# Performance work log

Measured on AMD Instinct MI355X. Metric: run time of the kernel, lower is better.

Reference implementation:

```python
import jax, jax.numpy as jnp
import numpy as np

# Structural hyperparams (mirror init_kwargs)
G, Q, C, D = 2, 8, 1024, 8          # groups, quantizers/group, codebook_size, codebook_dim
DIMS = 1024                          # residual_fsq.dim
DPG = DIMS // G                      # dim per group (project_out output)
B, L = 4, 4096                       # batch, frame length
UP_K, UP_S = 4, 2                    # upsample ConvTranspose1d kernel/stride
HEAD_K, HEAD_OUT = 7, 512            # head Conv1d kernel / out channels


def setup_inputs() -> dict:
    key = jax.random.key(0)
    ks = jax.random.split(key, 8)
    indices = jax.random.randint(ks[0], (B, G * Q, L), 0, C, dtype=jnp.int64)
    codebooks = jax.random.normal(ks[1], (G, Q, C, D), jnp.float32)
    scales = jax.random.uniform(ks[2], (G, Q, D), jnp.float32, 0.5, 2.0)
    W_out = jax.random.normal(ks[3], (G, D, DPG), jnp.float32) * (1.0 / np.sqrt(D))
    b_out = jnp.zeros((G, DPG), jnp.float32)
    W_up = jax.random.normal(ks[4], (DIMS, DIMS, UP_K), jnp.float32) * 0.02   # IOH layout
    b_up = jnp.zeros((DIMS,), jnp.float32)
    W_head = jax.random.normal(ks[5], (HEAD_OUT, DIMS, HEAD_K), jnp.float32) * 0.02  # OIH
    b_head = jnp.zeros((HEAD_OUT,), jnp.float32)
    return dict(indices=indices, codebooks=codebooks, scales=scales,
                W_out=W_out, b_out=b_out, W_up=W_up, b_up=b_up,
                W_head=W_head, b_head=b_head)


def reference(indices, codebooks, scales, W_out, b_out, W_up, b_up, W_head, b_head):
    b, gq, l = indices.shape
    g, q = codebooks.shape[0], codebooks.shape[1]
    # [B, G*Q, L] -> [G, B, L, Q]  (matches view + permute in forward)
    idx = indices.reshape(b, g, q, l).transpose(1, 0, 3, 2)
    mask = idx == -1                              # dropout-padded codes
    idx0 = jnp.where(mask, 0, idx)
    # gather codes per (group, quantizer): codebooks[g, q, idx0[g,b,l,q]] -> [G,B,L,Q,D]
    g_ix = jnp.arange(g)[:, None, None, None]
    q_ix = jnp.arange(q)[None, None, None, :]
    codes = codebooks[g_ix, q_ix, idx0]
    # mask, scale, sum over quantizers (residual sum)
    codes = jnp.where(mask[..., None], 0.0, codes) * scales[:, None, None, :, :]
    summed = codes.sum(axis=3)                    # [G,B,L,D]
    # per-group project_out: Linear(D -> DPG)
    z = jnp.einsum('gbld,gde->gble', summed, W_out) + b_out[:, None, None, :]
    # concat groups along feature dim -> [B, L, DIMS], then NCH for convs
    z_q = z.transpose(1, 2, 0, 3).reshape(b, l, g * z.shape[-1])
    zc = z_q.transpose(0, 2, 1)                   # [B, DIMS, L]
    # upsample: ConvTranspose1d(DIMS->DIMS, k=4, stride=2) -> [B, DIMS, 2L]
    zu = jax.lax.conv_transpose(zc, W_up, strides=(UP_S,), padding='SAME',
                                dimension_numbers=('NCH', 'IOH', 'NCH'))
    zu = zu + b_up[None, :, None]
    # head: Conv1d(DIMS -> HEAD_OUT, k=7, same padding)
    x = jax.lax.conv_general_dilated(zu, W_head, window_strides=(1,), padding='SAME',
                                     dimension_numbers=('NCH', 'OIH', 'NCH'))
    x = x + b_head[None, :, None]
    return x
```

## Files before the change

### kernel.cpp

```cpp
#include <hip/hip_runtime.h>
#include <hip/hip_bf16.h>

typedef __attribute__((ext_vector_type(8))) short bf16x8;
typedef __attribute__((ext_vector_type(4))) float f32x4;

#define GQ 16
#define L_IN 4096
#define T_UP 8192
#define CB 1024
#define ZROWS 4098
#define UROWS 8198

__device__ __forceinline__ void gload16(const void* g, void* l) {
    __builtin_amdgcn_global_load_lds((const __attribute__((address_space(1))) void*)g,
                                     (__attribute__((address_space(3))) void*)l, 16, 0, 0);
}

#define SB()  __builtin_amdgcn_s_barrier()
#define LGKM() do { asm volatile("s_waitcnt lgkmcnt(0)" ::: "memory"); \
                    __builtin_amdgcn_sched_barrier(0); } while (0)
#define VMW(n) do { __builtin_amdgcn_sched_barrier(0); \
                    asm volatile("s_waitcnt vmcnt(" #n ")" ::: "memory"); \
                    __builtin_amdgcn_sched_barrier(0); } while (0)

#define MM(MH, NH) do {                                                          \
    __builtin_amdgcn_s_setprio(1);                                               \
    _Pragma("unroll") for (int j_ = 0; j_ < 4; ++j_)                             \
      _Pragma("unroll") for (int n_ = 0; n_ < 2; ++n_)                           \
        _Pragma("unroll") for (int s_ = 0; s_ < 2; ++s_)                         \
          acc[(MH)*4 + j_][(NH)*2 + n_] = __builtin_amdgcn_mfma_f32_16x16x32_bf16( \
              af[j_][s_], bq[(NH)*2 + n_][s_], acc[(MH)*4 + j_][(NH)*2 + n_],    \
              0, 0, 0);                                                          \
    __builtin_amdgcn_s_setprio(0);                                               \
} while (0)

__global__ __launch_bounds__(256) void zero_pads(__hip_bfloat16* __restrict__ zp,
                                                 __hip_bfloat16* __restrict__ zup) {
    int idx = blockIdx.x * 256 + threadIdx.x;
    if (idx < 8192) {
        int b = idx >> 11, rs = (idx >> 10) & 1, c = idx & 1023;
        size_t row = (size_t)b * ZROWS + (rs ? (ZROWS - 1) : 0);
        zp[row * 1024 + c] = __float2bfloat16(0.f);
    } else if (idx < 8192 + 24576) {
        int rem = idx - 8192;
        int b = rem / 6144, r2 = rem % 6144;
        int r6 = r2 >> 10, c = r2 & 1023;
        size_t row = (size_t)b * UROWS + (r6 < 3 ? r6 : (UROWS - 6 + r6));
        zup[row * 1024 + c] = __float2bfloat16(0.f);
    }
}

__global__ __launch_bounds__(256) void repack_up(const float* __restrict__ Wup,
                                                 __hip_bfloat16* __restrict__ Wr) {
    int idx = blockIdx.x * 256 + threadIdx.x;
    int kk = idx >> 20;
    int co = (idx >> 10) & 1023;
    int ci = idx & 1023;
    Wr[idx] = __float2bfloat16(Wup[((ci << 10) + co) * 4 + kk]);
}

__global__ __launch_bounds__(256) void repack_head(const float* __restrict__ Wh,
                                                   __hip_bfloat16* __restrict__ Wr) {
    int idx = blockIdx.x * 256 + threadIdx.x;
    int kk = idx >> 19;
    int rem = idx & ((1 << 19) - 1);
    int o = rem >> 10;
    int ci = rem & 1023;
    Wr[idx] = __float2bfloat16(Wh[(o * 1024 + ci) * 7 + kk]);
}

__global__ __launch_bounds__(256) void dequant_project(
    const int* __restrict__ indices, const float* __restrict__ codebooks,
    const float* __restrict__ scales, const float* __restrict__ Wout,
    const float* __restrict__ bout, __hip_bfloat16* __restrict__ z)
{
    __shared__ float w_lds[8192];
    __shared__ float b_lds[1024];
    __shared__ float part[128];
    __shared__ float summed[16];
    int tid = threadIdx.x;
    for (int k = tid; k < 8192; k += 256) w_lds[k] = Wout[k];
    for (int k = tid; k < 1024; k += 256) b_lds[k] = bout[k];
    int p0 = blockIdx.x * 16;
    int b  = p0 >> 12;
    int l0 = p0 & 4095;
    __syncthreads();
    for (int i = 0; i < 16; ++i) {
        int l = l0 + i;
        if (tid < 128) {
            int gq = tid >> 3;
            int d  = tid & 7;
            int idx = indices[(b * GQ + gq) * L_IN + l];
            float v = 0.f;
            if (idx >= 0) {
                int ic = (idx < CB) ? idx : 0;
                v = codebooks[(gq * CB + ic) * 8 + d] * scales[gq * 8 + d];
            }
            part[tid] = v;
        }
        __syncthreads();
        if (tid < 16) {
            int g = tid >> 3, d = tid & 7;
            float s = 0.f;
            for (int q = 0; q < 8; ++q) s += part[(g * 8 + q) * 8 + d];
            summed[tid] = s;
        }
        __syncthreads();
        #pragma unroll
        for (int j = 0; j < 4; ++j) {
            int c = tid + j * 256;
            int g = c >> 9;
            float acc = b_lds[c];
            #pragma unroll
            for (int d = 0; d < 8; ++d)
                acc += summed[g * 8 + d] * w_lds[(g * 8 + d) * 512 + (c & 511)];
            z[((size_t)b * ZROWS + l + 1) * 1024 + c] = __float2bfloat16(acc);
        }
        __syncthreads();
    }
}


__global__ __launch_bounds__(512, 2) void conv_up_mfma(
    const __hip_bfloat16* __restrict__ zp, const __hip_bfloat16* __restrict__ Wr,
    const float* __restrict__ bup, __hip_bfloat16* __restrict__ zup)
{
    __shared__ __hip_bfloat16 Als[2][256][64];
    __shared__ __hip_bfloat16 Bls[2][256][64];
    const int tid = threadIdx.x;
    const int lane = tid & 63;
    const int w = tid >> 6;
    const int wm = w >> 2, wn = w & 3;
    const int l15 = lane & 15, kq = lane >> 4;
    const int m0  = blockIdx.x * 256;
    const int co0 = blockIdx.y * 256;
    const int b = blockIdx.z >> 1, P = blockIdx.z & 1;
    const int NT = 32, NIT = 16;

    const __hip_bfloat16* abase = zp + ((size_t)b * ZROWS + m0 + P) * 1024;
    const __hip_bfloat16* bbase = Wr + ((size_t)P * 1024 + co0) * 1024;

    auto stage = [&](int kt, int part) {
        if (kt >= NT) return;
        const int buf = kt & 1;
        const int j = kt >> 4, ci0 = (kt & 15) << 6;
        const int rb = (part & 1) << 7;
        const __hip_bfloat16* src;
        __hip_bfloat16* dst;
        if (part < 2) { src = abase + ((size_t)j + rb) * 1024 + ci0;
                        dst = &Als[buf][rb][0]; }
        else          { src = bbase + ((size_t)j * 2048 + rb) * 1024 + ci0;
                        dst = &Bls[buf][rb][0]; }
        #pragma unroll
        for (int it = 0; it < 2; ++it) {
            int chunk = it * 512 + tid;
            int row = chunk >> 3, cs = chunk & 7;
            int cq = cs ^ (row & 7);
            gload16(src + (size_t)row * 1024 + cq * 8,
                    (char*)dst + ((it * 512 + (w << 6)) << 4));
        }
    };

    f32x4 acc[8][4];
    const f32x4 z4 = {0.f, 0.f, 0.f, 0.f};
    #pragma unroll
    for (int i = 0; i < 8; ++i)
        #pragma unroll
        for (int j = 0; j < 4; ++j) acc[i][j] = z4;

    bf16x8 af[4][2], bq[4][2];

    auto rdA = [&](int buf, int mh) {
        #pragma unroll
        for (int j = 0; j < 4; ++j)
            #pragma unroll
            for (int sl = 0; sl < 2; ++sl) {
                int row = (wm << 7) + (mh << 6) + j * 16 + l15;
                int ch = (sl * 4 + kq) ^ (row & 7);
                af[j][sl] = *(const bf16x8*)&Als[buf][row][ch * 8];
            }
    };
    auto rdB = [&](int buf) {
        #pragma unroll
        for (int nf = 0; nf < 4; ++nf)
            #pragma unroll
            for (int sl = 0; sl < 2; ++sl) {
                int row = (wn << 6) + nf * 16 + l15;
                int ch = (sl * 4 + kq) ^ (row & 7);
                bq[nf][sl] = *(const bf16x8*)&Bls[buf][row][ch * 8];
            }
    };

    stage(0, 2); stage(0, 3); stage(0, 0); stage(0, 1);
    stage(1, 2); stage(1, 3); stage(1, 0);
    VMW(6);
    SB();

    for (int it = 0; it < NIT; ++it) {
        const bool lastit = (it == NIT - 1);
        rdA(0, 0); rdB(0);
        stage(2 * it + 1, 1);
        SB(); LGKM(); MM(0, 0); SB();
        stage(2 * it + 2, 2);
        SB(); MM(0, 1); SB();
        rdA(0, 1);
        stage(2 * it + 2, 3);
        SB(); LGKM(); MM(1, 1); SB();
        stage(2 * it + 2, 0);
        if (lastit) { VMW(0); } else { VMW(6); }
        SB(); MM(1, 0); SB();
        rdA(1, 0); rdB(1);
        stage(2 * it + 2, 1);
        SB(); LGKM(); MM(0, 0); SB();
        stage(2 * it + 3, 2);
        SB(); MM(0, 1); SB();
        rdA(1, 1);
        stage(2 * it + 3, 3);
        SB(); LGKM(); MM(1, 1); SB();
        stage(2 * it + 3, 0);
        if (!lastit) { VMW(6); }
        SB(); MM(1, 0); SB();
    }

    float bias[4];
    #pragma unroll
    for (int nf = 0; nf < 4; ++nf) bias[nf] = bup[co0 + (wn << 6) + nf * 16 + l15];
    const int mbase = m0 + (wm << 7) + (kq << 2);
    const int cob = co0 + (wn << 6) + l15;
    #pragma unroll
    for (int mf = 0; mf < 8; ++mf)
        #pragma unroll
        for (int e = 0; e < 4; ++e) {
            int m = mbase + mf * 16 + e;
            size_t rowoff = ((size_t)b * UROWS + 3 + P + 2 * m) * 1024;
            #pragma unroll
            for (int nf = 0; nf < 4; ++nf)
                zup[rowoff + cob + nf * 16] = __float2bfloat16(acc[mf][nf][e] + bias[nf]);
        }
}

__global__ __launch_bounds__(512, 2) void conv_head_mfma(
    const __hip_bfloat16* __restrict__ zup, const __hip_bfloat16* __restrict__ Wr,
    const float* __restrict__ bh, float* __restrict__ out)
{
    __shared__ __hip_bfloat16 Als[2][256][64];
    __shared__ __hip_bfloat16 Bls[2][256][64];
    const int tid = threadIdx.x;
    const int lane = tid & 63;
    const int w = tid >> 6;
    const int wm = w >> 2, wn = w & 3;
    const int l15 = lane & 15, kq = lane >> 4;
    const int t0 = blockIdx.x * 256;
    const int o0 = blockIdx.y * 256;
    const int b  = blockIdx.z;
    const int NT = 112, NIT = 56;

    const __hip_bfloat16* bbase = zup + ((size_t)b * UROWS + t0) * 1024;

    auto stage = [&](int kt, int part) {
        if (kt >= NT) return;
        const int buf = kt & 1;
        const int kk = kt >> 4, ci0 = (kt & 15) << 6;
        const int rb = (part & 1) << 7;
        const __hip_bfloat16* src;
        __hip_bfloat16* dst;
        if (part < 2) { src = Wr + ((size_t)(kk * 512 + o0 + rb)) * 1024 + ci0;
                        dst = &Als[buf][rb][0]; }
        else          { src = bbase + ((size_t)(kk + rb)) * 1024 + ci0;
                        dst = &Bls[buf][rb][0]; }
        #pragma unroll
        for (int it = 0; it < 2; ++it) {
            int chunk = it * 512 + tid;
            int row = chunk >> 3, cs = chunk & 7;
            int cq = cs ^ (row & 7);
            gload16(src + (size_t)row * 1024 + cq * 8,
                    (char*)dst + ((it * 512 + (w << 6)) << 4));
        }
    };

    f32x4 acc[8][4];
    const f32x4 z4 = {0.f, 0.f, 0.f, 0.f};
    #pragma unroll
    for (int i = 0; i < 8; ++i)
        #pragma unroll
        for (int j = 0; j < 4; ++j) acc[i][j] = z4;

    bf16x8 af[4][2], bq[4][2];

    auto rdA = [&](int buf, int mh) {
        #pragma unroll
        for (int j = 0; j < 4; ++j)
            #pragma unroll
            for (int sl = 0; sl < 2; ++sl) {
                int row = (wm << 7) + (mh << 6) + j * 16 + l15;
                int ch = (sl * 4 + kq) ^ (row & 7);
                af[j][sl] = *(const bf16x8*)&Als[buf][row][ch * 8];
            }
    };
    auto rdB = [&](int buf) {
        #pragma unroll
        for (int nf = 0; nf < 4; ++nf)
            #pragma unroll
            for (int sl = 0; sl < 2; ++sl) {
                int row = (wn << 6) + nf * 16 + l15;
                int ch = (sl * 4 + kq) ^ (row & 7);
                bq[nf][sl] = *(const bf16x8*)&Bls[buf][row][ch * 8];
            }
    };

    stage(0, 2); stage(0, 3); stage(0, 0); stage(0, 1);
    stage(1, 2); stage(1, 3); stage(1, 0);
    VMW(6);
    SB();

    for (int it = 0; it < NIT; ++it) {
        const bool lastit = (it == NIT - 1);
        rdA(0, 0); rdB(0);
        stage(2 * it + 1, 1);
        SB(); LGKM(); MM(0, 0); SB();
        stage(2 * it + 2, 2);
        SB(); MM(0, 1); SB();
        rdA(0, 1);
        stage(2 * it + 2, 3);
        SB(); LGKM(); MM(1, 1); SB();
        stage(2 * it + 2, 0);
        if (lastit) { VMW(0); } else { VMW(6); }
        SB(); MM(1, 0); SB();
        rdA(1, 0); rdB(1);
        stage(2 * it + 2, 1);
        SB(); LGKM(); MM(0, 0); SB();
        stage(2 * it + 3, 2);
        SB(); MM(0, 1); SB();
        rdA(1, 1);
        stage(2 * it + 3, 3);
        SB(); LGKM(); MM(1, 1); SB();
        stage(2 * it + 3, 0);
        if (!lastit) { VMW(6); }
        SB(); MM(1, 0); SB();
    }

    const int obase = o0 + (wm << 7) + (kq << 2);
    const int tbase = t0 + (wn << 6) + l15;
    #pragma unroll
    for (int mf = 0; mf < 8; ++mf)
        #pragma unroll
        for (int e = 0; e < 4; ++e) {
            int o = obase + mf * 16 + e;
            float bias = bh[o];
            size_t rowoff = ((size_t)b * 512 + o) * T_UP + tbase;
            #pragma unroll
            for (int nf = 0; nf < 4; ++nf)
                out[rowoff + nf * 16] = acc[mf][nf][e] + bias;
        }
}

extern "C" void kernel_launch(void* const* d_in, const int* in_sizes, int n_in,
                              void* d_out, int out_size, void* d_ws, size_t ws_size,
                              hipStream_t stream) {
    const int*   indices   = (const int*)d_in[0];
    const float* codebooks = (const float*)d_in[1];
    const float* scales    = (const float*)d_in[2];
    const float* Wout      = (const float*)d_in[3];
    const float* bout      = (const float*)d_in[4];
    const float* Wup       = (const float*)d_in[5];
    const float* bup       = (const float*)d_in[6];
    const float* Wh        = (const float*)d_in[7];
    const float* bh        = (const float*)d_in[8];
    float* out = (float*)d_out;

    __hip_bfloat16* zp    = (__hip_bfloat16*)d_ws;
    __hip_bfloat16* zup   = zp + (size_t)4 * ZROWS * 1024;
    __hip_bfloat16* wr_up = zup + (size_t)4 * UROWS * 1024;
    __hip_bfloat16* wr_h  = wr_up + (size_t)4 * 1024 * 1024;

    zero_pads  <<<dim3(128),   dim3(256), 0, stream>>>(zp, zup);
    repack_up  <<<dim3(16384), dim3(256), 0, stream>>>(Wup, wr_up);
    repack_head<<<dim3(14336), dim3(256), 0, stream>>>(Wh, wr_h);
    dequant_project<<<dim3(1024), dim3(256), 0, stream>>>(indices, codebooks, scales,
                                                          Wout, bout, zp);
    conv_up_mfma  <<<dim3(16, 4, 8), dim3(512), 0, stream>>>(zp, wr_up, bup, zup);
    conv_head_mfma<<<dim3(32, 2, 4), dim3(512), 0, stream>>>(zup, wr_h, bh, out);
}
```

Before: 466.6 us.

## Interleave LDS fragment reads with MFMA phases in both conv GEMM loops

Splits the B-fragment LDS reads into low and high halves and issues the next fragment reads right after each MFMA block, inside the barrier window, instead of before the block that needs them. The intent is to overlap LDS read latency with matrix-core work in the upsample and head GEMM loops. Barriers are wrapped in compiler scheduling fences so the compiler cannot move memory operations across them. This adds scheduling constraints and register-liveness pressure, and there is a risk of reading LDS data while another wave is still overwriting it.

```diff
diff --git a/kernel.cpp b/kernel.cpp
--- a/kernel.cpp
+++ b/kernel.cpp
@@ -16,7 +16,11 @@
                                      (__attribute__((address_space(3))) void*)l, 16, 0, 0);
 }
 
-#define SB()  __builtin_amdgcn_s_barrier()
+#define SBR() do { asm volatile("" ::: "memory");                 \
+                   __builtin_amdgcn_sched_barrier(0);             \
+                   __builtin_amdgcn_s_barrier();                  \
+                   __builtin_amdgcn_sched_barrier(0);             \
+                   asm volatile("" ::: "memory"); } while (0)
 #define LGKM() do { asm volatile("s_waitcnt lgkmcnt(0)" ::: "memory"); \
                     __builtin_amdgcn_sched_barrier(0); } while (0)
 #define VMW(n) do { __builtin_amdgcn_sched_barrier(0); \
@@ -180,9 +184,19 @@
                 af[j][sl] = *(const bf16x8*)&Als[buf][row][ch * 8];
             }
     };
-    auto rdB = [&](int buf) {
-        #pragma unroll
-        for (int nf = 0; nf < 4; ++nf)
+    auto rdBlo = [&](int buf) {
+        #pragma unroll
+        for (int nf = 0; nf < 2; ++nf)
+            #pragma unroll
+            for (int sl = 0; sl < 2; ++sl) {
+                int row = (wn << 6) + nf * 16 + l15;
+                int ch = (sl * 4 + kq) ^ (row & 7);
+                bq[nf][sl] = *(const bf16x8*)&Bls[buf][row][ch * 8];
+            }
+    };
+    auto rdBhi = [&](int buf) {
+        #pragma unroll
+        for (int nf = 2; nf < 4; ++nf)
             #pragma unroll
             for (int sl = 0; sl < 2; ++sl) {
                 int row = (wn << 6) + nf * 16 + l15;
@@ -194,32 +208,51 @@
     stage(0, 2); stage(0, 3); stage(0, 0); stage(0, 1);
     stage(1, 2); stage(1, 3); stage(1, 0);
     VMW(6);
-    SB();
+    SBR();
+    rdA(0, 0); rdBlo(0);
 
     for (int it = 0; it < NIT; ++it) {
         const bool lastit = (it == NIT - 1);
-        rdA(0, 0); rdB(0);
         stage(2 * it + 1, 1);
-        SB(); LGKM(); MM(0, 0); SB();
+        SBR(); LGKM();
+        MM(0, 0);
+        rdBhi(0);
+        SBR();
         stage(2 * it + 2, 2);
-        SB(); MM(0, 1); SB();
+        SBR(); LGKM();
+        MM(0, 1);
         rdA(0, 1);
+        SBR();
         stage(2 * it + 2, 3);
-        SB(); LGKM(); MM(1, 1); SB();
+        SBR(); LGKM();
+        MM(1, 1);
+        SBR();
         stage(2 * it + 2, 0);
         if (lastit) { VMW(0); } else { VMW(6); }
-        SB(); MM(1, 0); SB();
-        rdA(1, 0); rdB(1);
+        SBR();
+        MM(1, 0);
+        rdA(1, 0); rdBlo(1);
+        SBR();
         stage(2 * it + 2, 1);
-        SB(); LGKM(); MM(0, 0); SB();
+        SBR(); LGKM();
+        MM(0, 0);
+        rdBhi(1);
+        SBR();
         stage(2 * it + 3, 2);
-        SB(); MM(0, 1); SB();
+        SBR(); LGKM();
+        MM(0, 1);
         rdA(1, 1);
+        SBR();
         stage(2 * it + 3, 3);
-        SB(); LGKM(); MM(1, 1); SB();
+        SBR(); LGKM();
+        MM(1, 1);
+        SBR();
         stage(2 * it + 3, 0);
         if (!lastit) { VMW(6); }
-        SB(); MM(1, 0); SB();
+        SBR();
+        MM(1, 0);
+        if (!lastit) { rdA(0, 0); rdBlo(0); }
+        SBR();
     }
 
     float bias[4];
@@ -297,9 +330,19 @@
                 af[j][sl] = *(const bf16x8*)&Als[buf][row][ch * 8];
             }
     };
-    auto rdB = [&](int buf) {
-        #pragma unroll
-        for (int nf = 0; nf < 4; ++nf)
+    auto rdBlo = [&](int buf) {
+        #pragma unroll
+        for (int nf = 0; nf < 2; ++nf)
+            #pragma unroll
+            for (int sl = 0; sl < 2; ++sl) {
+                int row = (wn << 6) + nf * 16 + l15;
+                int ch = (sl * 4 + kq) ^ (row & 7);
+                bq[nf][sl] = *(const bf16x8*)&Bls[buf][row][ch * 8];
+            }
+    };
+    auto rdBhi = [&](int buf) {
+        #pragma unroll
+        for (int nf = 2; nf < 4; ++nf)
             #pragma unroll
             for (int sl = 0; sl < 2; ++sl) {
                 int row = (wn << 6) + nf * 16 + l15;
@@ -311,32 +354,51 @@
     stage(0, 2); stage(0, 3); stage(0, 0); stage(0, 1);
     stage(1, 2); stage(1, 3); stage(1, 0);
     VMW(6);
-    SB();
+    SBR();
+    rdA(0, 0); rdBlo(0);
 
     for (int it = 0; it < NIT; ++it) {
         const bool lastit = (it == NIT - 1);
-        rdA(0, 0); rdB(0);
         stage(2 * it + 1, 1);
-        SB(); LGKM(); MM(0, 0); SB();
+        SBR(); LGKM();
+        MM(0, 0);
+        rdBhi(0);
+        SBR();
         stage(2 * it + 2, 2);
-        SB(); MM(0, 1); SB();
+        SBR(); LGKM();
+        MM(0, 1);
         rdA(0, 1);
+        SBR();
         stage(2 * it + 2, 3);
-        SB(); LGKM(); MM(1, 1); SB();
+        SBR(); LGKM();
+        MM(1, 1);
+        SBR();
         stage(2 * it + 2, 0);
         if (lastit) { VMW(0); } else { VMW(6); }
-        SB(); MM(1, 0); SB();
-        rdA(1, 0); rdB(1);
+        SBR();
+        MM(1, 0);
+        rdA(1, 0); rdBlo(1);
+        SBR();
         stage(2 * it + 2, 1);
-        SB(); LGKM(); MM(0, 0); SB();
+        SBR(); LGKM();
+        MM(0, 0);
+        rdBhi(1);
+        SBR();
         stage(2 * it + 3, 2);
-        SB(); MM(0, 1); SB();
+        SBR(); LGKM();
+        MM(0, 1);
         rdA(1, 1);
+        SBR();
         stage(2 * it + 3, 3);
-        SB(); LGKM(); MM(1, 1); SB();
+        SBR(); LGKM();
+        MM(1, 1);
+        SBR();
         stage(2 * it + 3, 0);
         if (!lastit) { VMW(6); }
-        SB(); MM(1, 0); SB();
+        SBR();
+        MM(1, 0);
+        if (!lastit) { rdA(0, 0); rdBlo(0); }
+        SBR();
     }
 
     const int obase = o0 + (wm << 7) + (kq << 2);
```

New measurement: 466.7 us. About the same (+0.0%).
